# Performance work log

Measured on AMD Instinct MI355X. Metric: run time of the kernel, lower is better.

The kernel has to match this reference:

```python
import jax, jax.numpy as jnp
import numpy as np
from jax import lax

B, INP, OUP, H, W = 16, 128, 128, 56, 56
EXPAND = 6
HID = INP * EXPAND  # 768
EPS = 1e-5


def setup_inputs() -> dict:
    key = jax.random.key(0)
    ks = jax.random.split(key, 18)
    x = jax.random.normal(ks[0], (B, INP, H, W), dtype=jnp.float32)
    mask = jax.random.randint(ks[1], (B, 1, H, W), 0, 2, dtype=jnp.int32)
    w1 = jax.random.normal(ks[2], (HID, INP), dtype=jnp.float32) * 0.05
    g1 = 1.0 + 0.1 * jax.random.normal(ks[3], (HID,), dtype=jnp.float32)
    b1 = 0.1 * jax.random.normal(ks[4], (HID,), dtype=jnp.float32)
    m1 = 0.1 * jax.random.normal(ks[5], (HID,), dtype=jnp.float32)
    v1 = jax.random.uniform(ks[6], (HID,), dtype=jnp.float32) + 0.5
    wdw = jax.random.normal(ks[7], (HID, 1, 3, 3), dtype=jnp.float32) * 0.05
    g2 = 1.0 + 0.1 * jax.random.normal(ks[8], (HID,), dtype=jnp.float32)
    b2 = 0.1 * jax.random.normal(ks[9], (HID,), dtype=jnp.float32)
    m2 = 0.1 * jax.random.normal(ks[10], (HID,), dtype=jnp.float32)
    v2 = jax.random.uniform(ks[11], (HID,), dtype=jnp.float32) + 0.5
    w2 = jax.random.normal(ks[12], (OUP, HID), dtype=jnp.float32) * 0.05
    g3 = 1.0 + 0.1 * jax.random.normal(ks[13], (OUP,), dtype=jnp.float32)
    b3 = 0.1 * jax.random.normal(ks[14], (OUP,), dtype=jnp.float32)
    m3 = 0.1 * jax.random.normal(ks[15], (OUP,), dtype=jnp.float32)
    v3 = jax.random.uniform(ks[16], (OUP,), dtype=jnp.float32) + 0.5
    return dict(x=x, w1=w1, g1=g1, b1=b1, m1=m1, v1=v1, wdw=wdw,
                g2=g2, b2=b2, m2=m2, v2=v2, w2=w2,
                g3=g3, b3=b3, m3=m3, v3=v3, mask=mask)


def _bn(h, g, b, m, v):
    # inference-mode BatchNorm2d: (h - mean) * gamma/sqrt(var+eps) + beta
    scale = g / jnp.sqrt(v + EPS)
    return (h - m[None, :, None, None]) * scale[None, :, None, None] + b[None, :, None, None]


def reference(x, w1, g1, b1, m1, v1, wdw, g2, b2, m2, v2, w2, g3, b3, m3, v3, mask):
    mf = mask.astype(x.dtype)  # [B,1,H,W] binary mask ('std')
    # mask_dilate: 3x3 binary dilation (dilate_stride=1) so the depthwise conv
    # has valid neighbors for every active output pixel
    md = lax.reduce_window(mf, 0.0, lax.max, (1, 1, 3, 3), (1, 1, 1, 1), 'SAME')
    # expand 1x1 conv + BN + ReLU6, restricted to dilated mask
    h = jnp.einsum('bchw,kc->bkhw', x, w1)            # [B,HID,H,W]
    h = jnp.clip(_bn(h, g1, b1, m1, v1), 0.0, 6.0) * md
    # depthwise 3x3 conv + BN + ReLU6, restricted to std mask
    h = lax.conv_general_dilated(h, wdw, (1, 1), 'SAME',
                                 feature_group_count=HID,
                                 dimension_numbers=('NCHW', 'OIHW', 'NCHW'))
    h = jnp.clip(_bn(h, g2, b2, m2, v2), 0.0, 6.0) * mf
    # project 1x1 conv + BN (no relu), restricted to std mask
    h = jnp.einsum('bkhw,ok->bohw', h, w2)            # [B,OUP,H,W]
    h = _bn(h, g3, b3, m3, v3) * mf
    # scatter-add into identity path
    return x + h
```

## Files before the change

### kernel.cpp

```cpp
#include <hip/hip_runtime.h>
#include <hip/hip_bf16.h>

#define BATCH 16
#define INP   128
#define OUP   128
#define HH    56
#define WW    56
#define HWSZ  3136
#define HID   768
#define EPSV  1e-5f

#define CPST  265
#define H2STR 72
#define XSTR  130
#define H1ROW 64
#define H1RPC 58

typedef __attribute__((ext_vector_type(8))) short bf16x8;
typedef __attribute__((ext_vector_type(4))) float f32x4;
typedef __attribute__((ext_vector_type(2))) float f32x2;
typedef __attribute__((address_space(1))) const unsigned GU;
typedef __attribute__((address_space(3))) unsigned LU;

__device__ __forceinline__ unsigned short f2b(float f) {
    unsigned u = __float_as_uint(f);
    return (unsigned short)((u + 0x7FFFu + ((u >> 16) & 1u)) >> 16);
}
__device__ __forceinline__ float blo(unsigned u){ return __uint_as_float(u << 16); }
__device__ __forceinline__ float bhi(unsigned u){ return __uint_as_float(u & 0xFFFF0000u); }
__device__ __forceinline__ unsigned pkbf(float lo, float hi) {
    unsigned r;
    asm("v_cvt_pk_bf16_f32 %0, %1, %2" : "=v"(r) : "v"(lo), "v"(hi));
    return r;
}
__device__ __forceinline__ void pkfma(f32x2& a, f32x2 b, f32x2 c) {
    asm("v_pk_fma_f32 %0, %1, %2, %0" : "+v"(a) : "v"(b), "v"(c));
}

__global__ void prep(const float* __restrict__ w1, const float* __restrict__ g1,
                     const float* __restrict__ b1, const float* __restrict__ m1, const float* __restrict__ v1,
                     const float* __restrict__ wdw, const float* __restrict__ g2,
                     const float* __restrict__ b2, const float* __restrict__ m2, const float* __restrict__ v2,
                     const float* __restrict__ w2, const float* __restrict__ g3,
                     const float* __restrict__ b3, const float* __restrict__ m3, const float* __restrict__ v3,
                     const int* __restrict__ mask,
                     unsigned short* __restrict__ w1f, unsigned short* __restrict__ w2f,
                     float* __restrict__ be1o, float* __restrict__ wdsf,
                     float* __restrict__ be2o, float* __restrict__ be3o,
                     float* __restrict__ mdf, float* __restrict__ mff,
                     unsigned* __restrict__ h1p)
{
    int gid = blockIdx.x * blockDim.x + threadIdx.x;
    int stp = gridDim.x * blockDim.x;
    for (int i = gid; i < HID * INP; i += stp) {
        int r = i >> 7, k = i & 127;
        float s = g1[r] * rsqrtf(v1[r] + EPSV);
        int ht = r >> 4, r16 = r & 15, ks = k >> 5, g = (k >> 3) & 3, e = k & 7;
        w1f[((((ht * 4 + ks) * 4 + g) * 16 + r16) << 3) + e] = f2b(w1[i] * s);
    }
    for (int i = gid; i < OUP * HID; i += stp) {
        int r = i / HID, k = i - r * HID;
        float s = g3[r] * rsqrtf(v3[r] + EPSV);
        int ot = r >> 4, r16 = r & 15, ch = k >> 6, ks = (k >> 5) & 1, g = (k >> 3) & 3, e = k & 7;
        int lane = g * 16 + r16;
        w2f[((((ot * 12 + ch) * 2 + ks) * 64 + lane) << 3) + e] = f2b(w2[i] * s);
    }
    for (int i = gid; i < HID; i += stp) {
        float s1 = g1[i] * rsqrtf(v1[i] + EPSV);
        be1o[i] = b1[i] - m1[i] * s1;
        float s2 = g2[i] * rsqrtf(v2[i] + EPSV);
        be2o[i] = b2[i] - m2[i] * s2;
    }
    for (int i = gid; i < HID * 9; i += stp) {
        int q = i / HID, c = i - q * HID;
        float s2 = g2[c] * rsqrtf(v2[c] + EPSV);
        wdsf[i] = wdw[c * 9 + q] * s2;
    }
    for (int i = gid; i < OUP; i += stp) {
        float s3 = g3[i] * rsqrtf(v3[i] + EPSV);
        be3o[i] = b3[i] - m3[i] * s3;
    }
    for (int i = gid; i < BATCH * HWSZ; i += stp) {
        int b = i / HWSZ, p = i - b * HWSZ;
        int y = p / WW, xx = p - y * WW;
        float mf = (float)mask[i];
        float md = 0.f;
        for (int dy = -1; dy <= 1; ++dy)
            for (int dx = -1; dx <= 1; ++dx) {
                int yy = y + dy, xc = xx + dx;
                if (yy >= 0 && yy < HH && xc >= 0 && xc < WW)
                    md = fmaxf(md, (float)mask[b * HWSZ + yy * WW + xc]);
            }
        mff[i] = mf;
        mdf[i] = md;
    }
    for (int i = gid; i < BATCH * 384 * 2 * H1ROW; i += stp) {
        int rr = i >> 6, d = i & 63;
        int bcp = rr >> 1, side = rr & 1;
        h1p[((size_t)bcp * H1RPC + (side ? 57 : 0)) * H1ROW + d] = 0;
    }
    for (int i = gid; i < BATCH * 384 * 56 * 8; i += stp) {
        int rr = i >> 3, d = i & 7;
        h1p[((size_t)(rr / 56) * H1RPC + 1 + (rr % 56)) * H1ROW + (d < 4 ? d : 56 + d)] = 0;
    }
}

__launch_bounds__(512, 4)
__global__ void k1_expand(const float* __restrict__ x,
                          const unsigned short* __restrict__ w1f,
                          const float* __restrict__ be1g,
                          const float* __restrict__ mdf,
                          unsigned* __restrict__ h1p)
{
    __shared__ unsigned short xs[128 * XSTR];
    const int t = threadIdx.x, lane = t & 63, wv = t >> 6;
    const int g = lane >> 4, r16 = lane & 15;
    const int pid = blockIdx.x;
    const int l = (pid & 7) * 150 + (pid >> 3);
    const int hb = l % 3;
    const int pb = (l / 3) % 25;
    const int b  = l / 75;
    const int p0 = pb * 128;
    const int whid = wv & 3;
    const int wpx  = wv >> 2;

    for (int rep = 0; rep < 8; ++rep) {
        int id = t + rep * 512;
        int px = id & 127, c4 = id >> 7;
        int p = p0 + px;
        ushort4 u; u.x = 0; u.y = 0; u.z = 0; u.w = 0;
        if (p < HWSZ) {
            const float* xp = x + ((size_t)(b * INP + c4 * 4)) * HWSZ + p;
            unsigned lo = pkbf(xp[0], xp[HWSZ]);
            unsigned hi = pkbf(xp[2 * HWSZ], xp[3 * HWSZ]);
            u.x = (unsigned short)lo; u.y = (unsigned short)(lo >> 16);
            u.z = (unsigned short)hi; u.w = (unsigned short)(hi >> 16);
        }
        *(ushort4*)&xs[px * XSTR + (((c4 >> 1) ^ (px & 15)) << 3) + ((c4 & 1) << 2)] = u;
    }
    __syncthreads();

    f32x4 acc[4][4];
    #pragma unroll
    for (int mt = 0; mt < 4; ++mt)
        #pragma unroll
        for (int nt = 0; nt < 4; ++nt) {
            acc[mt][nt][0] = 0.f; acc[mt][nt][1] = 0.f;
            acc[mt][nt][2] = 0.f; acc[mt][nt][3] = 0.f;
        }
    const int hbase = hb * 256 + whid * 64;
    const int htb = hbase >> 4;

    #pragma unroll
    for (int ks = 0; ks < 4; ++ks) {
        bf16x8 af[4];
        #pragma unroll
        for (int mt = 0; mt < 4; ++mt)
            af[mt] = *(const bf16x8*)&w1f[((((htb + mt) * 4 + ks) * 64) + lane) << 3];
        #pragma unroll
        for (int nt = 0; nt < 4; ++nt) {
            int px = wpx * 64 + nt * 16 + r16;
            bf16x8 bf = *(const bf16x8*)&xs[px * XSTR + (((ks * 4 + g) ^ r16) << 3)];
            #pragma unroll
            for (int mt = 0; mt < 4; ++mt)
                acc[mt][nt] = __builtin_amdgcn_mfma_f32_16x16x32_bf16(af[mt], bf, acc[mt][nt], 0, 0, 0);
        }
    }

    #pragma unroll
    for (int nt = 0; nt < 4; ++nt) {
        const int pg = p0 + wpx * 64 + nt * 16;
        if (pg >= HWSZ) continue;
        const int p = pg + r16;
        const int row = (p * 9363) >> 19;
        const int col = p - row * 56;
        const float md = mdf[b * HWSZ + p];
        #pragma unroll
        for (int mt = 0; mt < 4; ++mt) {
            const float4 be4 = *(const float4*)&be1g[hbase + mt * 16 + g * 4];
            f32x4 a = acc[mt][nt];
            float v0 = fminf(fmaxf(a[0] + be4.x, 0.f), 6.f) * md;
            float v1 = fminf(fmaxf(a[1] + be4.y, 0.f), 6.f) * md;
            float v2 = fminf(fmaxf(a[2] + be4.z, 0.f), 6.f) * md;
            float v3 = fminf(fmaxf(a[3] + be4.w, 0.f), 6.f) * md;
            const int c2 = (hbase >> 1) + mt * 8 + g * 2;
            const size_t ad = ((size_t)(b * 384 + c2) * H1RPC + row + 1) * H1ROW + 4 + col;
            h1p[ad] = pkbf(v0, v1);
            h1p[ad + H1RPC * H1ROW] = pkbf(v2, v3);
        }
    }
}

__launch_bounds__(512, 4)
__global__ void k23(const unsigned* __restrict__ h1p,
                    const unsigned short* __restrict__ w2f,
                    const float* __restrict__ wdsf,
                    const float* __restrict__ be2g,
                    const float* __restrict__ be3g,
                    const float* __restrict__ mff,
                    const float* __restrict__ x,
                    float* __restrict__ out)
{
    __shared__ unsigned stg[32 * CPST];
    __shared__ unsigned short h2s[112 * H2STR];
    __shared__ float mfv_[112];

    const int t = threadIdx.x, lane = t & 63, wv = t >> 6;
    const int g = lane >> 4, r16 = lane & 15;
    const int pid = blockIdx.x;
    const int l = (pid & 7) * 56 + (pid >> 3);
    const int strip = l % 28, b = l / 28;
    const int y0 = strip * 2, p0 = strip * 112;

    if (t < 112) mfv_[t] = mff[b * HWSZ + p0 + t];

    const unsigned* gb[4];
    unsigned* lb[4];
    #pragma unroll
    for (int i = 0; i < 4; ++i) {
        const int cpw = wv * 4 + i;
        gb[i] = h1p + (((size_t)(b * 384 + cpw) * H1RPC + y0) << 6) + lane * 4;
        lb[i] = &stg[cpw * CPST];
    }
    auto dma = [&](int ch) {
        #pragma unroll
        for (int i = 0; i < 4; ++i)
            __builtin_amdgcn_global_load_lds((GU*)(gb[i] + (size_t)ch * 32 * H1RPC * H1ROW),
                                             (LU*)lb[i], 16, 0, 0);
    };

    const int cp_c = t & 31, row2 = (t >> 5) & 1, q = t >> 6;
    unsigned* const h2d = (unsigned*)h2s;

    auto phaseDW = [&](int ch) {
        f32x2 acc2[7];
        {
            const float2 be2 = *(const float2*)&be2g[ch * 64 + 2 * cp_c];
            #pragma unroll
            for (int j = 0; j < 7; ++j) { acc2[j][0] = be2.x; acc2[j][1] = be2.y; }
        }
        const int w0d = q * 7 + 3;
        #pragma unroll
        for (int dy = 0; dy < 3; ++dy) {
            f32x2 wt0 = *(const f32x2*)&wdsf[(dy * 3 + 0) * HID + ch * 64 + 2 * cp_c];
            f32x2 wt1 = *(const f32x2*)&wdsf[(dy * 3 + 1) * HID + ch * 64 + 2 * cp_c];
            f32x2 wt2 = *(const f32x2*)&wdsf[(dy * 3 + 2) * HID + ch * 64 + 2 * cp_c];
            const unsigned* rb = &stg[cp_c * CPST + (row2 + dy) * H1ROW + w0d];
            f32x2 p[9];
            #pragma unroll
            for (int k = 0; k < 9; ++k) {
                unsigned u = rb[k];
                p[k][0] = blo(u); p[k][1] = bhi(u);
            }
            #pragma unroll
            for (int j = 0; j < 7; ++j) {
                pkfma(acc2[j], p[j], wt0);
                pkfma(acc2[j], p[j + 1], wt1);
                pkfma(acc2[j], p[j + 2], wt2);
            }
        }
        #pragma unroll
        for (int j = 0; j < 7; ++j) {
            const int px = row2 * 56 + q * 7 + j;
            const float mv = mfv_[px];
            float vL = __builtin_amdgcn_fmed3f(acc2[j][0], 0.f, 6.f) * mv;
            float vH = __builtin_amdgcn_fmed3f(acc2[j][1], 0.f, 6.f) * mv;
            h2d[px * 36 + (((cp_c >> 2) ^ (px & 7)) << 2) + (cp_c & 3)] = pkbf(vL, vH);
        }
    };

    f32x4 pacc[8];
    #pragma unroll
    for (int ot = 0; ot < 8; ++ot) {
        pacc[ot][0] = 0.f; pacc[ot][1] = 0.f; pacc[ot][2] = 0.f; pacc[ot][3] = 0.f;
    }
    const int ppx = wv * 16 + r16;

    auto phaseP = [&](int ch) {
        if (wv < 7) {
            #pragma unroll
            for (int ks = 0; ks < 2; ++ks) {
                const bf16x8 hb = *(const bf16x8*)&h2s[ppx * H2STR + (((ks * 4 + g) ^ (ppx & 7)) << 3)];
                #pragma unroll
                for (int ot = 0; ot < 8; ++ot) {
                    const bf16x8 pw = *(const bf16x8*)&w2f[((((ot * 12 + ch) * 2 + ks) * 64) + lane) << 3];
                    pacc[ot] = __builtin_amdgcn_mfma_f32_16x16x32_bf16(pw, hb, pacc[ot], 0, 0, 0);
                }
            }
        }
    };

    dma(0);
    __syncthreads();
    for (int ch = 0; ch < 12; ++ch) {
        phaseDW(ch);
        __syncthreads();
        if (ch + 1 < 12) dma(ch + 1);
        phaseP(ch);
        __syncthreads();
    }

    if (wv < 7) {
        const float mv = mfv_[ppx];
        #pragma unroll
        for (int ot = 0; ot < 8; ++ot) {
            const int ob = ot * 16 + g * 4;
            const float4 be4 = *(const float4*)&be3g[ob];
            const size_t base = (size_t)(b * OUP + ob) * HWSZ + p0 + ppx;
            out[base]            = x[base]            + (pacc[ot][0] + be4.x) * mv;
            out[base + HWSZ]     = x[base + HWSZ]     + (pacc[ot][1] + be4.y) * mv;
            out[base + 2 * HWSZ] = x[base + 2 * HWSZ] + (pacc[ot][2] + be4.z) * mv;
            out[base + 3 * HWSZ] = x[base + 3 * HWSZ] + (pacc[ot][3] + be4.w) * mv;
        }
    }
}

extern "C" void kernel_launch(void* const* d_in, const int* in_sizes, int n_in,
                              void* d_out, int out_size, void* d_ws, size_t ws_size,
                              hipStream_t stream) {
    (void)in_sizes; (void)n_in; (void)out_size; (void)ws_size;
    const float* x   = (const float*)d_in[0];
    const float* w1  = (const float*)d_in[1];
    const float* g1  = (const float*)d_in[2];
    const float* b1  = (const float*)d_in[3];
    const float* m1  = (const float*)d_in[4];
    const float* v1  = (const float*)d_in[5];
    const float* wdw = (const float*)d_in[6];
    const float* g2  = (const float*)d_in[7];
    const float* b2  = (const float*)d_in[8];
    const float* m2  = (const float*)d_in[9];
    const float* v2  = (const float*)d_in[10];
    const float* w2  = (const float*)d_in[11];
    const float* g3  = (const float*)d_in[12];
    const float* b3  = (const float*)d_in[13];
    const float* m3  = (const float*)d_in[14];
    const float* v3  = (const float*)d_in[15];
    const int*  mask = (const int*)d_in[16];
    float* out = (float*)d_out;

    char* ws = (char*)d_ws;
    unsigned short* w1f = (unsigned short*)ws;
    unsigned short* w2f = (unsigned short*)(ws + 196608);
    float* be1o = (float*)(ws + 393216);
    float* wdsf = (float*)(ws + 396288);
    float* be2o = (float*)(ws + 423936);
    float* be3o = (float*)(ws + 427008);
    float* mdf  = (float*)(ws + 427520);
    float* mff  = (float*)(ws + 628224);
    unsigned* h1p = (unsigned*)(ws + 828928);

    prep<<<256, 256, 0, stream>>>(w1, g1, b1, m1, v1, wdw, g2, b2, m2, v2,
                                  w2, g3, b3, m3, v3, mask,
                                  w1f, w2f, be1o, wdsf, be2o, be3o, mdf, mff, h1p);
    k1_expand<<<dim3(1200), 512, 0, stream>>>(x, w1f, be1o, mdf, h1p);
    k23<<<dim3(448), 512, 0, stream>>>(h1p, w2f, wdsf, be2o, be3o, mff, x, out);
}
```

Before: 105.1 us.

## Widen k23 strips to four rows and hoist projection weights into registers

The fused depthwise+projection kernel now processes 4-row strips (224 pixels) per block instead of 2, halving the block count. This cuts redundant halo loads of the expanded activation and reuses each projection weight fragment across two pixel tiles per wave. Projection weights are loaded into registers once per channel chunk instead of per MFMA. The h2 swizzle is replaced with a padded stride, depthwise reads use vectorized uint2 loads, and the prep kernel now zeroes only the padding columns that are read, with wider stores. In exchange, register pressure rises, occupancy drops to 2 blocks per CU, and only 224 blocks are launched, so some CUs may be underused.

Measured after the change: 108.6 us. 1.03x slower.

```diff
diff --git a/kernel.cpp b/kernel.cpp
--- a/kernel.cpp
+++ b/kernel.cpp
@@ -10,8 +10,8 @@
 #define HID   768
 #define EPSV  1e-5f
 
-#define CPST  265
-#define H2STR 72
+#define CPST  521
+#define H2STR 66
 #define XSTR  130
 #define H1ROW 64
 #define H1RPC 58
@@ -94,14 +94,17 @@
         mff[i] = mf;
         mdf[i] = md;
     }
-    for (int i = gid; i < BATCH * 384 * 2 * H1ROW; i += stp) {
-        int rr = i >> 6, d = i & 63;
+    uint4 z4; z4.x = 0; z4.y = 0; z4.z = 0; z4.w = 0;
+    for (int i = gid; i < BATCH * 384 * 2 * 16; i += stp) {
+        int rr = i >> 4, q4 = i & 15;
         int bcp = rr >> 1, side = rr & 1;
-        h1p[((size_t)bcp * H1RPC + (side ? 57 : 0)) * H1ROW + d] = 0;
-    }
-    for (int i = gid; i < BATCH * 384 * 56 * 8; i += stp) {
-        int rr = i >> 3, d = i & 7;
-        h1p[((size_t)(rr / 56) * H1RPC + 1 + (rr % 56)) * H1ROW + (d < 4 ? d : 56 + d)] = 0;
+        *(uint4*)&h1p[((size_t)bcp * H1RPC + (side ? 57 : 0)) * H1ROW + q4 * 4] = z4;
+    }
+    for (int i = gid; i < BATCH * 384 * 56; i += stp) {
+        int bcp = i / 56, row = i - bcp * 56;
+        size_t base = ((size_t)bcp * H1RPC + 1 + row) * H1ROW;
+        h1p[base + 3] = 0;
+        h1p[base + 60] = 0;
     }
 }
 
@@ -191,7 +194,7 @@
     }
 }
 
-__launch_bounds__(512, 4)
+__launch_bounds__(512, 2)
 __global__ void k23(const unsigned* __restrict__ h1p,
                     const unsigned short* __restrict__ w2f,
                     const float* __restrict__ wdsf,
@@ -202,90 +205,120 @@
                     float* __restrict__ out)
 {
     __shared__ unsigned stg[32 * CPST];
-    __shared__ unsigned short h2s[112 * H2STR];
-    __shared__ float mfv_[112];
+    __shared__ unsigned short h2s[224 * H2STR];
+    __shared__ float mfv_[224];
 
     const int t = threadIdx.x, lane = t & 63, wv = t >> 6;
     const int g = lane >> 4, r16 = lane & 15;
     const int pid = blockIdx.x;
-    const int l = (pid & 7) * 56 + (pid >> 3);
-    const int strip = l % 28, b = l / 28;
-    const int y0 = strip * 2, p0 = strip * 112;
-
-    if (t < 112) mfv_[t] = mff[b * HWSZ + p0 + t];
+    const int l = (pid & 7) * 28 + (pid >> 3);
+    const int strip = l % 14, b = l / 14;
+    const int y0 = strip * 4, p0 = y0 * 56;
+    const int start = (y0 == 52) ? 50 : y0;
+    const int shift = y0 - start;
+
+    if (t < 224) mfv_[t] = mff[b * HWSZ + p0 + t];
 
     const unsigned* gb[4];
     unsigned* lb[4];
     #pragma unroll
     for (int i = 0; i < 4; ++i) {
         const int cpw = wv * 4 + i;
-        gb[i] = h1p + (((size_t)(b * 384 + cpw) * H1RPC + y0) << 6) + lane * 4;
+        gb[i] = h1p + (((size_t)(b * 384 + cpw) * H1RPC + start) << 6) + lane * 4;
         lb[i] = &stg[cpw * CPST];
     }
     auto dma = [&](int ch) {
-        #pragma unroll
-        for (int i = 0; i < 4; ++i)
-            __builtin_amdgcn_global_load_lds((GU*)(gb[i] + (size_t)ch * 32 * H1RPC * H1ROW),
-                                             (LU*)lb[i], 16, 0, 0);
+        const size_t co = (size_t)ch * 32 * H1RPC * H1ROW;
+        #pragma unroll
+        for (int i = 0; i < 4; ++i) {
+            __builtin_amdgcn_global_load_lds((GU*)(gb[i] + co), (LU*)lb[i], 16, 0, 0);
+            __builtin_amdgcn_global_load_lds((GU*)(gb[i] + co + 256), (LU*)(lb[i] + 256), 16, 0, 0);
+        }
     };
 
-    const int cp_c = t & 31, row2 = (t >> 5) & 1, q = t >> 6;
+    const int cp_c = t & 31;
+    const int rq = t >> 5, r4 = rq & 3, q = rq >> 2;
     unsigned* const h2d = (unsigned*)h2s;
+    bf16x8 pwreg[16];
+
+    auto loadPW = [&](int ch) {
+        #pragma unroll
+        for (int ot = 0; ot < 8; ++ot)
+            #pragma unroll
+            for (int ks = 0; ks < 2; ++ks)
+                pwreg[ot * 2 + ks] = *(const bf16x8*)&w2f[((((ot * 12 + ch) * 2 + ks) * 64) + lane) << 3];
+    };
 
     auto phaseDW = [&](int ch) {
-        f32x2 acc2[7];
+        f32x2 acc2[14];
         {
             const float2 be2 = *(const float2*)&be2g[ch * 64 + 2 * cp_c];
             #pragma unroll
-            for (int j = 0; j < 7; ++j) { acc2[j][0] = be2.x; acc2[j][1] = be2.y; }
-        }
-        const int w0d = q * 7 + 3;
+            for (int j = 0; j < 14; ++j) { acc2[j][0] = be2.x; acc2[j][1] = be2.y; }
+        }
         #pragma unroll
         for (int dy = 0; dy < 3; ++dy) {
             f32x2 wt0 = *(const f32x2*)&wdsf[(dy * 3 + 0) * HID + ch * 64 + 2 * cp_c];
             f32x2 wt1 = *(const f32x2*)&wdsf[(dy * 3 + 1) * HID + ch * 64 + 2 * cp_c];
             f32x2 wt2 = *(const f32x2*)&wdsf[(dy * 3 + 2) * HID + ch * 64 + 2 * cp_c];
-            const unsigned* rb = &stg[cp_c * CPST + (row2 + dy) * H1ROW + w0d];
-            f32x2 p[9];
-            #pragma unroll
-            for (int k = 0; k < 9; ++k) {
-                unsigned u = rb[k];
-                p[k][0] = blo(u); p[k][1] = bhi(u);
-            }
-            #pragma unroll
-            for (int j = 0; j < 7; ++j) {
+            const unsigned* rp = &stg[cp_c * CPST + (r4 + shift + dy) * H1ROW + 4 + q * 14];
+            f32x2 p[16];
+            {
+                unsigned u = rp[-1]; p[0][0] = blo(u); p[0][1] = bhi(u);
+            }
+            #pragma unroll
+            for (int i = 0; i < 7; ++i) {
+                uint2 d = *(const uint2*)(rp + 2 * i);
+                p[1 + 2 * i][0] = blo(d.x); p[1 + 2 * i][1] = bhi(d.x);
+                p[2 + 2 * i][0] = blo(d.y); p[2 + 2 * i][1] = bhi(d.y);
+            }
+            {
+                unsigned u = rp[14]; p[15][0] = blo(u); p[15][1] = bhi(u);
+            }
+            #pragma unroll
+            for (int j = 0; j < 14; ++j) {
                 pkfma(acc2[j], p[j], wt0);
                 pkfma(acc2[j], p[j + 1], wt1);
                 pkfma(acc2[j], p[j + 2], wt2);
             }
         }
         #pragma unroll
-        for (int j = 0; j < 7; ++j) {
-            const int px = row2 * 56 + q * 7 + j;
+        for (int j = 0; j < 14; ++j) {
+            const int px = r4 * 56 + q * 14 + j;
             const float mv = mfv_[px];
             float vL = __builtin_amdgcn_fmed3f(acc2[j][0], 0.f, 6.f) * mv;
             float vH = __builtin_amdgcn_fmed3f(acc2[j][1], 0.f, 6.f) * mv;
-            h2d[px * 36 + (((cp_c >> 2) ^ (px & 7)) << 2) + (cp_c & 3)] = pkbf(vL, vH);
+            h2d[px * 33 + cp_c] = pkbf(vL, vH);
         }
     };
 
-    f32x4 pacc[8];
-    #pragma unroll
-    for (int ot = 0; ot < 8; ++ot) {
-        pacc[ot][0] = 0.f; pacc[ot][1] = 0.f; pacc[ot][2] = 0.f; pacc[ot][3] = 0.f;
-    }
-    const int ppx = wv * 16 + r16;
-
-    auto phaseP = [&](int ch) {
-        if (wv < 7) {
-            #pragma unroll
-            for (int ks = 0; ks < 2; ++ks) {
-                const bf16x8 hb = *(const bf16x8*)&h2s[ppx * H2STR + (((ks * 4 + g) ^ (ppx & 7)) << 3)];
+    const int t0 = (wv < 6) ? 2 * wv : 12 + (wv - 6);
+    const bool has2 = wv < 6;
+    f32x4 pacc[2][8];
+    #pragma unroll
+    for (int ti = 0; ti < 2; ++ti)
+        #pragma unroll
+        for (int ot = 0; ot < 8; ++ot) {
+            pacc[ti][ot][0] = 0.f; pacc[ti][ot][1] = 0.f;
+            pacc[ti][ot][2] = 0.f; pacc[ti][ot][3] = 0.f;
+        }
+
+    auto phaseP = [&]() {
+        #pragma unroll
+        for (int ks = 0; ks < 2; ++ks) {
+            {
+                const int px = t0 * 16 + r16;
+                const bf16x8 hb = *(const bf16x8*)&h2s[px * H2STR + (ks * 4 + g) * 8];
                 #pragma unroll
-                for (int ot = 0; ot < 8; ++ot) {
-                    const bf16x8 pw = *(const bf16x8*)&w2f[((((ot * 12 + ch) * 2 + ks) * 64) + lane) << 3];
-                    pacc[ot] = __builtin_amdgcn_mfma_f32_16x16x32_bf16(pw, hb, pacc[ot], 0, 0, 0);
-                }
+                for (int ot = 0; ot < 8; ++ot)
+                    pacc[0][ot] = __builtin_amdgcn_mfma_f32_16x16x32_bf16(pwreg[ot * 2 + ks], hb, pacc[0][ot], 0, 0, 0);
+            }
+            if (has2) {
+                const int px = (2 * wv + 1) * 16 + r16;
+                const bf16x8 hb = *(const bf16x8*)&h2s[px * H2STR + (ks * 4 + g) * 8];
+                #pragma unroll
+                for (int ot = 0; ot < 8; ++ot)
+                    pacc[1][ot] = __builtin_amdgcn_mfma_f32_16x16x32_bf16(pwreg[ot * 2 + ks], hb, pacc[1][ot], 0, 0, 0);
             }
         }
     };
@@ -293,24 +326,28 @@
     dma(0);
     __syncthreads();
     for (int ch = 0; ch < 12; ++ch) {
+        loadPW(ch);
         phaseDW(ch);
         __syncthreads();
         if (ch + 1 < 12) dma(ch + 1);
-        phaseP(ch);
+        phaseP();
         __syncthreads();
     }
 
-    if (wv < 7) {
-        const float mv = mfv_[ppx];
+    #pragma unroll
+    for (int ti = 0; ti < 2; ++ti) {
+        if (ti == 1 && !has2) break;
+        const int px = (ti == 0 ? t0 : 2 * wv + 1) * 16 + r16;
+        const float mv = mfv_[px];
         #pragma unroll
         for (int ot = 0; ot < 8; ++ot) {
             const int ob = ot * 16 + g * 4;
             const float4 be4 = *(const float4*)&be3g[ob];
-            const size_t base = (size_t)(b * OUP + ob) * HWSZ + p0 + ppx;
-            out[base]            = x[base]            + (pacc[ot][0] + be4.x) * mv;
-            out[base + HWSZ]     = x[base + HWSZ]     + (pacc[ot][1] + be4.y) * mv;
-            out[base + 2 * HWSZ] = x[base + 2 * HWSZ] + (pacc[ot][2] + be4.z) * mv;
-            out[base + 3 * HWSZ] = x[base + 3 * HWSZ] + (pacc[ot][3] + be4.w) * mv;
+            const size_t base = (size_t)(b * OUP + ob) * HWSZ + p0 + px;
+            out[base]            = x[base]            + (pacc[ti][ot][0] + be4.x) * mv;
+            out[base + HWSZ]     = x[base + HWSZ]     + (pacc[ti][ot][1] + be4.y) * mv;
+            out[base + 2 * HWSZ] = x[base + 2 * HWSZ] + (pacc[ti][ot][2] + be4.z) * mv;
+            out[base + 3 * HWSZ] = x[base + 3 * HWSZ] + (pacc[ti][ot][3] + be4.w) * mv;
         }
     }
 }
@@ -353,5 +390,5 @@
                                   w2, g3, b3, m3, v3, mask,
                                   w1f, w2f, be1o, wdsf, be2o, be3o, mdf, mff, h1p);
     k1_expand<<<dim3(1200), 512, 0, stream>>>(x, w1f, be1o, mdf, h1p);
-    k23<<<dim3(448), 512, 0, stream>>>(h1p, w2f, wdsf, be2o, be3o, mff, x, out);
-}
+    k23<<<dim3(224), 512, 0, stream>>>(h1p, w2f, wdsf, be2o, be3o, mff, x, out);
+}
```
